# Kernel tuning notes

Hardware: AMD Instinct MI355X
Metric: run time of the kernel (lower is better)

## Reference

```python
import jax, jax.numpy as jnp
import numpy as np

DIM = 1024
HEADS = 8
DIM_HEAD = 64
INNER = HEADS * DIM_HEAD  # 512


def setup_inputs() -> dict:
    key = jax.random.key(0)
    k1, k2, k3, k4 = jax.random.split(key, 4)
    x = jax.random.normal(k1, (4, 4096, DIM), dtype=jnp.float32)
    W_qkv = jax.random.normal(k2, (DIM, 3 * INNER), dtype=jnp.float32) * (DIM ** -0.5)
    W_out = jax.random.normal(k3, (INNER, DIM), dtype=jnp.float32) * (INNER ** -0.5)
    b_out = jax.random.normal(k4, (DIM,), dtype=jnp.float32) * 0.01
    return {"x": x, "W_qkv": W_qkv, "W_out": W_out, "b_out": b_out}


def reference(x, W_qkv, W_out, b_out):
    b, n, _ = x.shape
    qkv = x @ W_qkv                                   # [b, n, 3*inner]
    q, k, v = jnp.split(qkv, 3, axis=-1)              # each [b, n, inner]

    def to_heads(t):
        return t.reshape(b, n, HEADS, DIM_HEAD).transpose(0, 2, 1, 3)  # [b, h, n, d]

    q = jax.nn.elu(to_heads(q)) + 1.0
    k = jax.nn.elu(to_heads(k)) + 1.0
    v = to_heads(v)
    # kv summary matrix: [b, h, d, e]
    context = jnp.einsum('bhnd,bhne->bhde', k, v)
    out = jnp.einsum('bhde,bhnd->bhne', context, q)   # [b, h, n, e]
    out = out.transpose(0, 2, 1, 3).reshape(b, n, INNER)
    return out @ W_out + b_out
```

## Files before the change

kernel.cpp:

```cpp
#include <hip/hip_runtime.h>
#include <hip/hip_bf16.h>
#include <cstdint>

typedef __attribute__((ext_vector_type(4))) float f32x4;
typedef __attribute__((ext_vector_type(8))) short bf16x8;

__device__ __forceinline__ ushort f2bf(float f) {
  unsigned u = __builtin_bit_cast(unsigned, f);
  u += 0x7fffu + ((u >> 16) & 1u);
  return (ushort)(u >> 16);
}
__device__ __forceinline__ float bf2f(ushort h) {
  unsigned u = ((unsigned)h) << 16;
  return __builtin_bit_cast(float, u);
}

__device__ __forceinline__ void gload_lds16(const ushort* g, ushort* l) {
  __builtin_amdgcn_global_load_lds(
      (const __attribute__((address_space(1))) unsigned int*)g,
      (__attribute__((address_space(3))) unsigned int*)l, 16, 0, 0);
}

__device__ __forceinline__ void hard_barrier() {
  __builtin_amdgcn_sched_barrier(0);
  __builtin_amdgcn_s_barrier();
  __builtin_amdgcn_sched_barrier(0);
}

template <int N>
__device__ __forceinline__ void wait_vm() {
  if constexpr (N == 0) asm volatile("s_waitcnt vmcnt(0)" ::: "memory");
  else if constexpr (N == 3) asm volatile("s_waitcnt vmcnt(3)" ::: "memory");
  else if constexpr (N == 4) asm volatile("s_waitcnt vmcnt(4)" ::: "memory");
  else static_assert(N < 0, "unsupported vmcnt");
}

__global__ __launch_bounds__(256) void cvt_x_kernel(const float4* __restrict__ x,
                                                    ushort4* __restrict__ xb, int n4) {
  int stride = gridDim.x * blockDim.x;
  for (int i = blockIdx.x * blockDim.x + threadIdx.x; i < n4; i += stride) {
    float4 f = x[i];
    ushort4 o;
    o.x = f2bf(f.x); o.y = f2bf(f.y); o.z = f2bf(f.z); o.w = f2bf(f.w);
    xb[i] = o;
  }
}

__global__ __launch_bounds__(256) void transpose_w_kernel(const float* __restrict__ W,
                                                          ushort* __restrict__ Wt) {
  __shared__ float tile[32][33];
  int n0 = blockIdx.x * 32;
  int k0 = blockIdx.y * 32;
  int tx = threadIdx.x;
  int ty = threadIdx.y;
  #pragma unroll
  for (int p = 0; p < 4; ++p) {
    int k = k0 + ty + p * 8;
    tile[ty + p * 8][tx] = W[(size_t)k * 1536 + n0 + tx];
  }
  __syncthreads();
  #pragma unroll
  for (int p = 0; p < 4; ++p) {
    int n = n0 + ty + p * 8;
    Wt[(size_t)n * 1024 + k0 + tx] = f2bf(tile[tx][ty + p * 8]);
  }
}

template <int MREP, int LDA, int LDB, int NT>
__device__ __forceinline__ void gemm_core3(const ushort* __restrict__ A,
                                           const ushort* __restrict__ Bt,
                                           int row0, int col0, f32x4 acc[MREP][4],
                                           ushort* lds) {
  constexpr int BM = MREP * 32;
  constexpr int SLOT = (BM + 256) * 32;
  constexpr int ALOADS = BM / 128;
  constexpr int BLOADS = 2;
  constexpr int L = ALOADS + BLOADS;
  const int tid = threadIdx.x;
  const int l = tid & 63;
  const int wid = tid >> 6;
  const int fr = l & 15, fq = l >> 4;
  const int wr = wid >> 2, wc = wid & 3;

  const int g = tid >> 3;
  const int slotL = (tid & 7) ^ (g & 7);
  const int srow = 2 * g + (slotL >> 2);
  const int scol = (slotL & 3) * 8;
  const ushort* aSrc[ALOADS];
  const ushort* bSrc[BLOADS];
  #pragma unroll
  for (int p = 0; p < ALOADS; ++p)
    aSrc[p] = A + (size_t)(row0 + p * 128 + srow) * LDA + scol;
  #pragma unroll
  for (int p = 0; p < BLOADS; ++p)
    bSrc[p] = Bt + (size_t)(col0 + p * 128 + srow) * LDB + scol;

  auto stage = [&](int tt) {
    ushort* dst = lds + (tt % 3) * SLOT + tid * 8;
    const int ko = tt * 32;
    #pragma unroll
    for (int p = 0; p < ALOADS; ++p) gload_lds16(aSrc[p] + ko, dst + p * 4096);
    #pragma unroll
    for (int p = 0; p < BLOADS; ++p) gload_lds16(bSrc[p] + ko, dst + BM * 32 + p * 4096);
  };

  const int fsl = (((fr & 1) << 2) | fq) ^ (fr >> 1);
  const int frb = (fr >> 1) * 64 + fsl * 8;
  const int aOff = wr * (MREP * 512) + frb;
  const int bOff = BM * 32 + wc * 2048 + frb;

  auto compute = [&](int s) {
    const ushort* base = lds + s * SLOT;
    const ushort* aB = base + aOff;
    const ushort* bB = base + bOff;
    bf16x8 bv[4];
    #pragma unroll
    for (int n = 0; n < 4; ++n) bv[n] = *(const bf16x8*)(bB + n * 512);
    #pragma unroll
    for (int mh = 0; mh < MREP / 4; ++mh) {
      bf16x8 av[4];
      #pragma unroll
      for (int mm = 0; mm < 4; ++mm)
        av[mm] = *(const bf16x8*)(aB + (mh * 4 + mm) * 512);
      __builtin_amdgcn_s_setprio(1);
      #pragma unroll
      for (int mm = 0; mm < 4; ++mm)
        #pragma unroll
        for (int n = 0; n < 4; ++n)
          acc[mh * 4 + mm][n] =
              __builtin_amdgcn_mfma_f32_16x16x32_bf16(av[mm], bv[n], acc[mh * 4 + mm][n], 0, 0, 0);
      __builtin_amdgcn_s_setprio(0);
    }
  };

  stage(0);
  stage(1);
  wait_vm<L>();
  hard_barrier();
  for (int t = 0; t < NT - 2; ++t) {
    stage(t + 2);
    compute(t % 3);
    wait_vm<L>();
    hard_barrier();
  }
  compute((NT - 2) % 3);
  wait_vm<0>();
  hard_barrier();
  compute((NT - 1) % 3);
}

__global__ __launch_bounds__(512, 2) void gemm_qkv_kernel(const ushort* __restrict__ xb,
                                                          const ushort* __restrict__ wt,
                                                          ushort* __restrict__ qkv) {
  __shared__ ushort lds[3 * 512 * 32];
  f32x4 acc[8][4] = {};
  const int row0 = blockIdx.x * 256;
  const int col0 = blockIdx.y * 256;
  gemm_core3<8, 1024, 1024, 32>(xb, wt, row0, col0, acc, lds);
  const int l = threadIdx.x & 63;
  const int wid = threadIdx.x >> 6;
  const int wr = wid >> 2, wc = wid & 3;
  const int fr = l & 15, fq = l >> 4;
  #pragma unroll
  for (int m = 0; m < 8; ++m) {
    #pragma unroll
    for (int n = 0; n < 4; ++n) {
      const int c = col0 + wc * 64 + n * 16 + fr;
      #pragma unroll
      for (int j = 0; j < 4; ++j) {
        const int r = row0 + wr * 128 + m * 16 + fq * 4 + j;
        float v = acc[m][n][j];
        if (c < 1024) v = (v > 0.f) ? (v + 1.f) : __expf(v);
        qkv[(size_t)r * 1536 + c] = f2bf(v);
      }
    }
  }
}

__global__ __launch_bounds__(256) void ctx_kernel(const ushort* __restrict__ qkv,
                                                  float* __restrict__ part) {
  const int bh = blockIdx.x;
  const int split = blockIdx.y;
  const int b = bh >> 3, h = bh & 7;
  const int t = threadIdx.x;
  const int d0 = (t >> 4) * 4;
  const int e0 = (t & 15) * 4;
  __shared__ ushort ks[64][64];
  __shared__ ushort vs[64][64];
  float acc[4][4] = {};
  const int rowBase = b * 4096 + split * 256;
  for (int chunk = 0; chunk < 256; chunk += 64) {
    __syncthreads();
    #pragma unroll
    for (int p = 0; p < 2; ++p) {
      const int r = (t >> 3) + p * 32;
      const int c = (t & 7) * 8;
      const ushort* src = qkv + (size_t)(rowBase + chunk + r) * 1536;
      *(uint4*)&ks[r][c] = *(const uint4*)(src + 512 + h * 64 + c);
      *(uint4*)&vs[r][c] = *(const uint4*)(src + 1024 + h * 64 + c);
    }
    __syncthreads();
    for (int r = 0; r < 64; ++r) {
      ushort4 ku = *(const ushort4*)&ks[r][d0];
      ushort4 vu = *(const ushort4*)&vs[r][e0];
      float kk[4] = {bf2f(ku.x), bf2f(ku.y), bf2f(ku.z), bf2f(ku.w)};
      float vv[4] = {bf2f(vu.x), bf2f(vu.y), bf2f(vu.z), bf2f(vu.w)};
      #pragma unroll
      for (int i = 0; i < 4; ++i)
        #pragma unroll
        for (int j = 0; j < 4; ++j)
          acc[i][j] += kk[i] * vv[j];
    }
  }
  float* dst = part + ((size_t)split * 32 + bh) * 4096;
  #pragma unroll
  for (int i = 0; i < 4; ++i)
    #pragma unroll
    for (int j = 0; j < 4; ++j)
      dst[(d0 + i) * 64 + (e0 + j)] = acc[i][j];
}

__global__ __launch_bounds__(256) void ctx_reduce_kernel(const float* __restrict__ part,
                                                         float* __restrict__ ctx) {
  const int i = blockIdx.x * 256 + threadIdx.x;
  float s = 0.f;
  #pragma unroll
  for (int sp = 0; sp < 16; ++sp) s += part[(size_t)sp * 131072 + i];
  ctx[i] = s;
}

__global__ __launch_bounds__(256) void weff_kernel(const float* __restrict__ ctx,
                                                   const float* __restrict__ Wout,
                                                   ushort* __restrict__ weff) {
  const int bh = blockIdx.x;
  const int h = bh & 7;
  const int m0 = blockIdx.y * 128;
  const int t = threadIdx.x;
  __shared__ float cs[64 * 64];
  __shared__ float ws[64][128];
  #pragma unroll
  for (int p = 0; p < 4; ++p) {
    const int idx = p * 1024 + t * 4;
    *(float4*)&cs[idx] = *(const float4*)&ctx[(size_t)bh * 4096 + idx];
  }
  #pragma unroll
  for (int p = 0; p < 8; ++p) {
    const int e = (t >> 5) + p * 8;
    const int c = (t & 31) * 4;
    *(float4*)&ws[e][c] = *(const float4*)&Wout[(size_t)(h * 64 + e) * 1024 + m0 + c];
  }
  __syncthreads();
  const int m = t & 127;
  const int dh = (t >> 7) * 32;
  float acc[32] = {};
  for (int e = 0; e < 64; ++e) {
    const float w = ws[e][m];
    #pragma unroll
    for (int i = 0; i < 32; ++i)
      acc[i] += cs[(dh + i) * 64 + e] * w;
  }
  ushort* dst = weff + ((size_t)(bh >> 3) * 1024 + m0 + m) * 512 + h * 64 + dh;
  #pragma unroll
  for (int i = 0; i < 32; ++i) dst[i] = f2bf(acc[i]);
}

__global__ __launch_bounds__(512, 2) void gemm_out_kernel(const ushort* __restrict__ qkv,
                                                          const ushort* __restrict__ weff,
                                                          const float* __restrict__ bout,
                                                          float* __restrict__ out) {
  __shared__ ushort lds[3 * 512 * 32];
  f32x4 acc[8][4] = {};
  const int row0 = blockIdx.x * 256;
  const int col0 = blockIdx.y * 256;
  const int b = row0 >> 12;
  gemm_core3<8, 1536, 512, 16>(qkv, weff + (size_t)b * 1024 * 512, row0, col0, acc, lds);
  const int l = threadIdx.x & 63;
  const int wid = threadIdx.x >> 6;
  const int wr = wid >> 2, wc = wid & 3;
  const int fr = l & 15, fq = l >> 4;
  #pragma unroll
  for (int m = 0; m < 8; ++m) {
    #pragma unroll
    for (int n = 0; n < 4; ++n) {
      const int c = col0 + wc * 64 + n * 16 + fr;
      const float bb = bout[c];
      #pragma unroll
      for (int j = 0; j < 4; ++j) {
        const int r = row0 + wr * 128 + m * 16 + fq * 4 + j;
        out[(size_t)r * 1024 + c] = acc[m][n][j] + bb;
      }
    }
  }
}

extern "C" void kernel_launch(void* const* d_in, const int* in_sizes, int n_in,
                              void* d_out, int out_size, void* d_ws, size_t ws_size,
                              hipStream_t stream) {
  const float* x    = (const float*)d_in[0];
  const float* Wqkv = (const float*)d_in[1];
  const float* Wout = (const float*)d_in[2];
  const float* bout = (const float*)d_in[3];
  float* out = (float*)d_out;
  char* ws = (char*)d_ws;

  ushort* xb   = (ushort*)(ws);
  ushort* wt   = (ushort*)(ws + 33554432);
  ushort* qkv  = (ushort*)(ws + 36700160);
  float*  part = (float* )(ws + 87031808);
  float*  ctx  = (float* )(ws + 95420416);
  ushort* weff = (ushort*)(ws + 95944704);

  cvt_x_kernel<<<2048, 256, 0, stream>>>((const float4*)x, (ushort4*)xb, 16384 * 1024 / 4);
  transpose_w_kernel<<<dim3(48, 32), dim3(32, 8), 0, stream>>>(Wqkv, wt);
  gemm_qkv_kernel<<<dim3(64, 6), 512, 0, stream>>>(xb, wt, qkv);
  ctx_kernel<<<dim3(32, 16), 256, 0, stream>>>(qkv, part);
  ctx_reduce_kernel<<<512, 256, 0, stream>>>(part, ctx);
  weff_kernel<<<dim3(32, 8), 256, 0, stream>>>(ctx, Wout, weff);
  gemm_out_kernel<<<dim3(64, 4), 512, 0, stream>>>(qkv, weff, bout, out);
}
```

Before: 152.9 us.

## Restructure GEMM core into double-buffered K=64 pipeline with grid swizzle

```diff
diff --git a/kernel.cpp b/kernel.cpp
--- a/kernel.cpp
+++ b/kernel.cpp
@@ -30,7 +30,6 @@
 template <int N>
 __device__ __forceinline__ void wait_vm() {
   if constexpr (N == 0) asm volatile("s_waitcnt vmcnt(0)" ::: "memory");
-  else if constexpr (N == 3) asm volatile("s_waitcnt vmcnt(3)" ::: "memory");
   else if constexpr (N == 4) asm volatile("s_waitcnt vmcnt(4)" ::: "memory");
   else static_assert(N < 0, "unsupported vmcnt");
 }
@@ -66,97 +65,108 @@
   }
 }
 
-template <int MREP, int LDA, int LDB, int NT>
-__device__ __forceinline__ void gemm_core3(const ushort* __restrict__ A,
+template <int LDA, int LDB, int NT>
+__device__ __forceinline__ void gemm_core8(const ushort* __restrict__ A,
                                            const ushort* __restrict__ Bt,
-                                           int row0, int col0, f32x4 acc[MREP][4],
+                                           int row0, int col0, f32x4 acc[8][4],
                                            ushort* lds) {
-  constexpr int BM = MREP * 32;
-  constexpr int SLOT = (BM + 256) * 32;
-  constexpr int ALOADS = BM / 128;
-  constexpr int BLOADS = 2;
-  constexpr int L = ALOADS + BLOADS;
   const int tid = threadIdx.x;
   const int l = tid & 63;
   const int wid = tid >> 6;
   const int fr = l & 15, fq = l >> 4;
   const int wr = wid >> 2, wc = wid & 3;
 
-  const int g = tid >> 3;
-  const int slotL = (tid & 7) ^ (g & 7);
-  const int srow = 2 * g + (slotL >> 2);
-  const int scol = (slotL & 3) * 8;
-  const ushort* aSrc[ALOADS];
-  const ushort* bSrc[BLOADS];
-  #pragma unroll
-  for (int p = 0; p < ALOADS; ++p)
-    aSrc[p] = A + (size_t)(row0 + p * 128 + srow) * LDA + scol;
-  #pragma unroll
-  for (int p = 0; p < BLOADS; ++p)
-    bSrc[p] = Bt + (size_t)(col0 + p * 128 + srow) * LDB + scol;
-
-  auto stage = [&](int tt) {
-    ushort* dst = lds + (tt % 3) * SLOT + tid * 8;
-    const int ko = tt * 32;
-    #pragma unroll
-    for (int p = 0; p < ALOADS; ++p) gload_lds16(aSrc[p] + ko, dst + p * 4096);
-    #pragma unroll
-    for (int p = 0; p < BLOADS; ++p) gload_lds16(bSrc[p] + ko, dst + BM * 32 + p * 4096);
+  const int srow = tid >> 2;
+  const int lam = (tid & 3) ^ ((tid >> 3) & 3);
+  const ushort* aG = A + (size_t)(row0 + srow) * LDA + lam * 8;
+  const ushort* bG = Bt + (size_t)(col0 + srow) * LDB + lam * 8;
+
+  auto stageA = [&](int tt, int kap) {
+    ushort* d = lds + (tt & 1) * 32768 + kap * 8192 + tid * 8;
+    const ushort* s = aG + tt * 64 + kap * 32;
+    gload_lds16(s, d);
+    gload_lds16(s + (size_t)128 * LDA, d + 4096);
   };
-
-  const int fsl = (((fr & 1) << 2) | fq) ^ (fr >> 1);
-  const int frb = (fr >> 1) * 64 + fsl * 8;
-  const int aOff = wr * (MREP * 512) + frb;
-  const int bOff = BM * 32 + wc * 2048 + frb;
-
-  auto compute = [&](int s) {
-    const ushort* base = lds + s * SLOT;
-    const ushort* aB = base + aOff;
-    const ushort* bB = base + bOff;
-    bf16x8 bv[4];
-    #pragma unroll
-    for (int n = 0; n < 4; ++n) bv[n] = *(const bf16x8*)(bB + n * 512);
-    #pragma unroll
-    for (int mh = 0; mh < MREP / 4; ++mh) {
-      bf16x8 av[4];
+  auto stageB = [&](int tt, int kap) {
+    ushort* d = lds + (tt & 1) * 32768 + 16384 + kap * 8192 + tid * 8;
+    const ushort* s = bG + tt * 64 + kap * 32;
+    gload_lds16(s, d);
+    gload_lds16(s + (size_t)128 * LDB, d + 4096);
+  };
+
+  const int sig = fq ^ ((fr >> 1) & 3);
+  const int aOff = wr * 4096 + fr * 32 + sig * 8;
+  const int bOff = 16384 + wc * 2048 + fr * 32 + sig * 8;
+
+  auto mfma16 = [&](const bf16x8 av[4], const bf16x8 bv[4], int mh) {
+    __builtin_amdgcn_s_setprio(1);
+    #pragma unroll
+    for (int mm = 0; mm < 4; ++mm)
       #pragma unroll
-      for (int mm = 0; mm < 4; ++mm)
-        av[mm] = *(const bf16x8*)(aB + (mh * 4 + mm) * 512);
-      __builtin_amdgcn_s_setprio(1);
-      #pragma unroll
-      for (int mm = 0; mm < 4; ++mm)
-        #pragma unroll
-        for (int n = 0; n < 4; ++n)
-          acc[mh * 4 + mm][n] =
-              __builtin_amdgcn_mfma_f32_16x16x32_bf16(av[mm], bv[n], acc[mh * 4 + mm][n], 0, 0, 0);
-      __builtin_amdgcn_s_setprio(0);
-    }
+      for (int n = 0; n < 4; ++n)
+        acc[mh * 4 + mm][n] =
+            __builtin_amdgcn_mfma_f32_16x16x32_bf16(av[mm], bv[n], acc[mh * 4 + mm][n], 0, 0, 0);
+    __builtin_amdgcn_s_setprio(0);
   };
 
-  stage(0);
-  stage(1);
-  wait_vm<L>();
+  stageA(0, 0); stageB(0, 0); stageA(0, 1); stageB(0, 1);
+  wait_vm<4>();
   hard_barrier();
-  for (int t = 0; t < NT - 2; ++t) {
-    stage(t + 2);
-    compute(t % 3);
-    wait_vm<L>();
+
+  for (int t = 0; t < NT; ++t) {
+    const ushort* sb = lds + (t & 1) * 32768;
+    const bool pre = (t + 1 < NT);
+    bf16x8 av[4], bv[4];
+
+    #pragma unroll
+    for (int mm = 0; mm < 4; ++mm) av[mm] = *(const bf16x8*)(sb + aOff + mm * 512);
+    #pragma unroll
+    for (int n = 0; n < 4; ++n) bv[n] = *(const bf16x8*)(sb + bOff + n * 512);
+    if (pre) stageA(t + 1, 0);
     hard_barrier();
-  }
-  compute((NT - 2) % 3);
-  wait_vm<0>();
-  hard_barrier();
-  compute((NT - 1) % 3);
-}
-
-__global__ __launch_bounds__(512, 2) void gemm_qkv_kernel(const ushort* __restrict__ xb,
+    mfma16(av, bv, 0);
+
+    #pragma unroll
+    for (int mm = 0; mm < 4; ++mm) av[mm] = *(const bf16x8*)(sb + aOff + 2048 + mm * 512);
+    if (pre) { stageB(t + 1, 0); wait_vm<4>(); } else { wait_vm<0>(); }
+    hard_barrier();
+    mfma16(av, bv, 1);
+
+    #pragma unroll
+    for (int mm = 0; mm < 4; ++mm) av[mm] = *(const bf16x8*)(sb + 8192 + aOff + mm * 512);
+    #pragma unroll
+    for (int n = 0; n < 4; ++n) bv[n] = *(const bf16x8*)(sb + 8192 + bOff + n * 512);
+    if (pre) stageA(t + 1, 1);
+    hard_barrier();
+    mfma16(av, bv, 0);
+
+    #pragma unroll
+    for (int mm = 0; mm < 4; ++mm) av[mm] = *(const bf16x8*)(sb + 8192 + aOff + 2048 + mm * 512);
+    if (pre) { stageB(t + 1, 1); wait_vm<4>(); }
+    hard_barrier();
+    mfma16(av, bv, 1);
+  }
+}
+
+__device__ __forceinline__ void swz_grid(int nx, int& bx, int& by) {
+  const int bid = blockIdx.x;
+  const int nwg = gridDim.x;
+  const int cpx = nwg >> 3;
+  const int swz = (bid & 7) * cpx + (bid >> 3);
+  by = swz / nx;
+  bx = swz - by * nx;
+}
+
+__global__ __launch_bounds__(512, 1) void gemm_qkv_kernel(const ushort* __restrict__ xb,
                                                           const ushort* __restrict__ wt,
                                                           ushort* __restrict__ qkv) {
-  __shared__ ushort lds[3 * 512 * 32];
+  __shared__ ushort lds[65536];
   f32x4 acc[8][4] = {};
-  const int row0 = blockIdx.x * 256;
-  const int col0 = blockIdx.y * 256;
-  gemm_core3<8, 1024, 1024, 32>(xb, wt, row0, col0, acc, lds);
+  int bx, by;
+  swz_grid(64, bx, by);
+  const int row0 = bx * 256;
+  const int col0 = by * 256;
+  gemm_core8<1024, 1024, 16>(xb, wt, row0, col0, acc, lds);
   const int l = threadIdx.x & 63;
   const int wid = threadIdx.x >> 6;
   const int wr = wid >> 2, wc = wid & 3;
@@ -264,16 +274,18 @@
   for (int i = 0; i < 32; ++i) dst[i] = f2bf(acc[i]);
 }
 
-__global__ __launch_bounds__(512, 2) void gemm_out_kernel(const ushort* __restrict__ qkv,
+__global__ __launch_bounds__(512, 1) void gemm_out_kernel(const ushort* __restrict__ qkv,
                                                           const ushort* __restrict__ weff,
                                                           const float* __restrict__ bout,
                                                           float* __restrict__ out) {
-  __shared__ ushort lds[3 * 512 * 32];
+  __shared__ ushort lds[65536];
   f32x4 acc[8][4] = {};
-  const int row0 = blockIdx.x * 256;
-  const int col0 = blockIdx.y * 256;
+  int bx, by;
+  swz_grid(64, bx, by);
+  const int row0 = bx * 256;
+  const int col0 = by * 256;
   const int b = row0 >> 12;
-  gemm_core3<8, 1536, 512, 16>(qkv, weff + (size_t)b * 1024 * 512, row0, col0, acc, lds);
+  gemm_core8<1536, 512, 8>(qkv, weff + (size_t)b * 1024 * 512, row0, col0, acc, lds);
   const int l = threadIdx.x & 63;
   const int wid = threadIdx.x >> 6;
   const int wr = wid >> 2, wc = wid & 3;
@@ -312,9 +324,9 @@
 
   cvt_x_kernel<<<2048, 256, 0, stream>>>((const float4*)x, (ushort4*)xb, 16384 * 1024 / 4);
   transpose_w_kernel<<<dim3(48, 32), dim3(32, 8), 0, stream>>>(Wqkv, wt);
-  gemm_qkv_kernel<<<dim3(64, 6), 512, 0, stream>>>(xb, wt, qkv);
+  gemm_qkv_kernel<<<384, 512, 0, stream>>>(xb, wt, qkv);
   ctx_kernel<<<dim3(32, 16), 256, 0, stream>>>(qkv, part);
   ctx_reduce_kernel<<<512, 256, 0, stream>>>(part, ctx);
   weff_kernel<<<dim3(32, 8), 256, 0, stream>>>(ctx, Wout, weff);
-  gemm_out_kernel<<<dim3(64, 4), 512, 0, stream>>>(qkv, weff, bout, out);
-}
+  gemm_out_kernel<<<256, 512, 0, stream>>>(qkv, weff, bout, out);
+}
```

After: 155.9 us. About the same (+2.0%).
